# Performance work log

Hardware: AMD Instinct MI355X
Metric: run time of the kernel (lower is better)

The kernel has to match this reference:

```python
import jax, jax.numpy as jnp
import numpy as np

WEIGHT_SCALE = 0.02  # matches torch.randn(...)*0.02 init

def setup_inputs() -> dict:
    key = jax.random.key(0)
    k1, k2, k3, k4 = jax.random.split(key, 4)
    B, D = 16384, 1024
    x_re = jax.random.normal(k1, (B, D), dtype=jnp.float32)
    x_im = jax.random.normal(k2, (B, D), dtype=jnp.float32)
    w_re = jax.random.normal(k3, (D, D), dtype=jnp.float32) * WEIGHT_SCALE
    w_im = jax.random.normal(k4, (D, D), dtype=jnp.float32) * WEIGHT_SCALE
    return {"x_re": x_re, "x_im": x_im, "w_re": w_re, "w_im": w_im}

def reference(x_re, x_im, w_re, w_im):
    x = jax.lax.complex(x_re, x_im)            # [B, D] complex64
    W = jax.lax.complex(w_re, w_im)            # [D, D] complex64
    # Skew-Hermitian part: A = W - W^H
    A = W - jnp.conj(W.T)
    D = W.shape[0]
    I = jnp.eye(D, dtype=W.dtype)
    # Cayley transform: U = (I - A)^{-1} (I + A)  (unitary)
    U = jnp.linalg.solve(I - A, I + A)
    # Original: x @ U.transpose(-1, -2) (plain transpose, no conj)
    return x @ U.T
```

## Files before the change

### kernel.cpp

```cpp
#include <hip/hip_runtime.h>
#include <hip/hip_bf16.h>

#define DD 1024
#define NB 16384
#define SZ (DD * DD)
#define CHB 256

typedef unsigned short u16;
typedef __attribute__((ext_vector_type(2))) float f32x2;
typedef __attribute__((ext_vector_type(4))) float f32x4;
typedef __attribute__((ext_vector_type(8))) short short8;
typedef __attribute__((ext_vector_type(4))) short short4v;

__device__ __forceinline__ u16 f32_bf16(float f) {
  unsigned u = __builtin_bit_cast(unsigned, f);
  u += 0x7FFFu + ((u >> 16) & 1u);
  return (u16)(u >> 16);
}
__device__ __forceinline__ float bf16_f32(u16 h) {
  unsigned u = ((unsigned)h) << 16;
  return __builtin_bit_cast(float, u);
}
__device__ __forceinline__ void gload16(const void* g, void* l) {
  __builtin_amdgcn_global_load_lds(
      (const __attribute__((address_space(1))) unsigned int*)g,
      (__attribute__((address_space(3))) unsigned int*)l, 16, 0, 0);
}

struct CArgs {
  const u16 *Ar[3], *Ai[3];
  const u16 *Br[3], *Bi[3];
  int nseg;
  float alpha, g1, g2, ddiag;
  const u16 *e1r, *e1i, *e2r, *e2i;
  u16 *hi_n_re, *hi_n_im, *lo_n_re, *lo_n_im;
  u16 *t1_re, *t1_im;
  u16 *t2_re, *t2_im;
  u16 *lt_re, *lt_im;
  int t_ldt;
  unsigned t1_xi;
  const float *cxr, *cxi; u16 *cxb;
  int cm0a, cm1a, cm0b, cm1b;
};

__global__ __launch_bounds__(256, 2) void zchain(CArgs g) {
  constexpr int SA = 64 * 32, SB = 64 * 32;
  constexpr int SLOT = 2 * SA + 2 * SB;
  __shared__ __align__(16) u16 smem[4 * SLOT];
  const int tid = threadIdx.x;

  if ((int)blockIdx.x >= CHB) {
    int nra = g.cm1a - g.cm0a;
    int tot = nra + (g.cm1b - g.cm0b);
    for (int r = (int)blockIdx.x - CHB; r < tot; r += 256) {
      int m = (r < nra) ? (g.cm0a + r) : (g.cm0b + r - nra);
      f32x4 v = ((const f32x4*)g.cxr)[m * 256 + tid];
      short4v s;
      #pragma unroll
      for (int e = 0; e < 4; ++e) s[e] = (short)f32_bf16(v[e]);
      ((short4v*)g.cxb)[m * 512 + tid] = s;
      f32x4 w = ((const f32x4*)g.cxi)[m * 256 + tid];
      #pragma unroll
      for (int e = 0; e < 4; ++e) s[e] = (short)f32_bf16(w[e]);
      ((short4v*)g.cxb)[m * 512 + 256 + tid] = s;
    }
    return;
  }

  const int lane = tid & 63, wave = tid >> 6;
  const int wr = wave >> 1, wc = wave & 1;
  const int l15 = lane & 15, lg = lane >> 4;

  const int lin = blockIdx.x;
  const int xcd = lin & 7, tt = lin >> 3;
  const int by = (xcd >> 1) * 4 + (tt >> 3);
  const int bx = (xcd & 1) * 8 + (tt & 7);
  const int m0 = by * 64, n0 = bx * 64;

  const int arow = tid >> 2, agc = tid & 3;
  const int offA = (m0 + arow) * DD + ((agc ^ ((arow >> 1) & 3)) * 8);
  const int offB = (n0 + arow) * DD + ((agc ^ ((arow >> 1) & 3)) * 8);
  const int ldsAB = tid * 8;

  const int slotR = lg ^ ((l15 >> 1) & 3);
  int frA[2], frB[2];
  #pragma unroll
  for (int mf = 0; mf < 2; ++mf)
    frA[mf] = (wr * 32 + mf * 16 + l15) * 32 + slotR * 8;
  #pragma unroll
  for (int nf = 0; nf < 2; ++nf)
    frB[nf] = (wc * 32 + nf * 16 + l15) * 32 + slotR * 8;

  const int nt = g.nseg * 32;

  auto ISSUE = [&](int b) {
    if (b >= nt) return;
    int s = b >> 5, kk = (b & 31) << 5;
    u16* base = smem + (b & 3) * SLOT;
    gload16(g.Ar[s] + offA + kk, base + ldsAB);
    gload16(g.Ai[s] + offA + kk, base + SA + ldsAB);
    gload16(g.Br[s] + offB + kk, base + 2 * SA + ldsAB);
    gload16(g.Bi[s] + offB + kk, base + 2 * SA + SB + ldsAB);
  };

  f32x4 accre[2][2] = {};
  f32x4 accim[2][2] = {};

  ISSUE(0); ISSUE(1);
  asm volatile("s_waitcnt vmcnt(0)" ::: "memory");
  __builtin_amdgcn_s_barrier();

  for (int b = 0; b < nt; b += 2) {
    ISSUE(b + 2); ISSUE(b + 3);

    #pragma unroll
    for (int half = 0; half < 2; ++half) {
      const u16* base = smem + ((b + half) & 3) * SLOT;
      short8 ar[2], ai[2], br[2], bi[2], bin[2];
      #pragma unroll
      for (int mf = 0; mf < 2; ++mf) {
        ar[mf] = *(const short8*)(base + frA[mf]);
        ai[mf] = *(const short8*)(base + SA + frA[mf]);
      }
      #pragma unroll
      for (int nf = 0; nf < 2; ++nf) {
        br[nf] = *(const short8*)(base + 2 * SA + frB[nf]);
        bi[nf] = *(const short8*)(base + 2 * SA + SB + frB[nf]);
        #pragma unroll
        for (int e = 0; e < 8; ++e) bin[nf][e] = (short)(bi[nf][e] ^ (short)0x8000);
      }
      __builtin_amdgcn_s_setprio(1);
      #pragma unroll
      for (int mf = 0; mf < 2; ++mf)
      #pragma unroll
      for (int nf = 0; nf < 2; ++nf) {
        accre[mf][nf] = __builtin_amdgcn_mfma_f32_16x16x32_bf16(ar[mf], br[nf],  accre[mf][nf], 0, 0, 0);
        accre[mf][nf] = __builtin_amdgcn_mfma_f32_16x16x32_bf16(ai[mf], bin[nf], accre[mf][nf], 0, 0, 0);
        accim[mf][nf] = __builtin_amdgcn_mfma_f32_16x16x32_bf16(ar[mf], bi[nf],  accim[mf][nf], 0, 0, 0);
        accim[mf][nf] = __builtin_amdgcn_mfma_f32_16x16x32_bf16(ai[mf], br[nf],  accim[mf][nf], 0, 0, 0);
      }
      __builtin_amdgcn_s_setprio(0);
    }

    if (b + 2 < nt) {
      asm volatile("s_waitcnt vmcnt(0)" ::: "memory");
      __builtin_amdgcn_s_barrier();
    }
  }

  u16 hre[2][2][4], hie[2][2][4], lre[2][2][4], lie[2][2][4];
  #pragma unroll
  for (int mf = 0; mf < 2; ++mf)
  #pragma unroll
  for (int nf = 0; nf < 2; ++nf)
  #pragma unroll
  for (int r = 0; r < 4; ++r) {
    int gr = m0 + wr * 32 + mf * 16 + lg * 4 + r;
    int gc = n0 + wc * 32 + nf * 16 + l15;
    size_t idx = (size_t)gr * DD + gc;
    float v = g.alpha * accre[mf][nf][r];
    float w = g.alpha * accim[mf][nf][r];
    if (g.e1r) { v += g.g1 * bf16_f32(g.e1r[idx]); w += g.g1 * bf16_f32(g.e1i[idx]); }
    if (g.e2r) { v += g.g2 * bf16_f32(g.e2r[idx]); w += g.g2 * bf16_f32(g.e2i[idx]); }
    if (gr == gc) v += g.ddiag;
    u16 h1 = f32_bf16(v); hre[mf][nf][r] = h1;
    u16 h2 = f32_bf16(w); hie[mf][nf][r] = h2;
    lre[mf][nf][r] = f32_bf16(v - bf16_f32(h1));
    lie[mf][nf][r] = f32_bf16(w - bf16_f32(h2));
    if (g.hi_n_re) { g.hi_n_re[idx] = h1; g.hi_n_im[idx] = h2; }
    if (g.lo_n_re) { g.lo_n_re[idx] = lre[mf][nf][r]; g.lo_n_im[idx] = lie[mf][nf][r]; }
  }

  auto bounce = [&](u16 (&vals)[2][2][4], u16* outp, unsigned xorm) {
    if (!outp) return;
    __syncthreads();
    #pragma unroll
    for (int mf = 0; mf < 2; ++mf)
    #pragma unroll
    for (int nf = 0; nf < 2; ++nf)
    #pragma unroll
    for (int r = 0; r < 4; ++r) {
      int row = wr * 32 + mf * 16 + lg * 4 + r;
      int col = wc * 32 + nf * 16 + l15;
      smem[row * 66 + col] = vals[mf][nf][r];
    }
    __syncthreads();
    {
      int col = tid & 63, mb = (tid >> 6) * 16;
      short8 s0, s1;
      #pragma unroll
      for (int j = 0; j < 8; ++j) s0[j] = (short)(smem[(mb + j) * 66 + col] ^ xorm);
      #pragma unroll
      for (int j = 0; j < 8; ++j) s1[j] = (short)(smem[(mb + 8 + j) * 66 + col] ^ xorm);
      u16* p = outp + (size_t)(n0 + col) * g.t_ldt + m0 + mb;
      *(short8*)p = s0; *(short8*)(p + 8) = s1;
    }
  };

  bounce(hre, g.t1_re, 0);
  bounce(hie, g.t1_im, g.t1_xi);
  bounce(hre, g.t2_re, 0);
  bounce(hie, g.t2_im, 0);
  bounce(lre, g.lt_re, 0);
  bounce(lie, g.lt_im, 0);
}

#define RG_SLOT2 (2 * 256 * 64)
#define RG_LDS_BYTES (2 * RG_SLOT2 * 2)
#define RG_TILES 32

__global__ __launch_bounds__(512, 2) void rgemm(
    const u16* __restrict__ A, const u16* __restrict__ B,
    float* __restrict__ out, int ostride, int ooff)
{
  extern __shared__ u16 smem[];
  const int tid = threadIdx.x, lane = tid & 63, wave = tid >> 6;
  const int wr = wave >> 2, wc = wave & 3;
  const int l15 = lane & 15, lg = lane >> 4;

  int bx, by;
  { int lin = blockIdx.y * gridDim.x + blockIdx.x;
    int orig = (lin & 7) * 32 + (lin >> 3);
    bx = orig & 3; by = orig >> 2; }
  const int m0 = by * 256, n0 = bx * 256;

  const u16* __restrict__ Abase = A + (size_t)m0 * 2048;
  const u16* __restrict__ Bbase = B + (size_t)n0 * 2048;

  int gofsA[2], gofsB[2], lofs[2];
  #pragma unroll
  for (int i = 0; i < 2; ++i) {
    int c = i * 512 + tid;
    int sub = c >> 3;
    int sl = (c & 7) ^ (sub & 7);
    int rowA = (sub & 63) + 128 * (sub >> 6);
    int rowB = (sub & 31) + 64 * (sub >> 5);
    gofsA[i] = rowA * 2048 + sl * 8;
    gofsB[i] = rowB * 2048 + sl * 8;
    lofs[i] = c * 8;
  }

  int raf[8], rbf[8];
  #pragma unroll
  for (int mf = 0; mf < 4; ++mf)
    #pragma unroll
    for (int k = 0; k < 2; ++k)
      raf[mf * 2 + k] = (wr * 64 + mf * 16 + l15) * 64 +
                        (((k * 4 + lg) ^ (l15 & 7)) * 8);
  #pragma unroll
  for (int nf = 0; nf < 2; ++nf)
    #pragma unroll
    for (int k = 0; k < 2; ++k)
      rbf[nf * 2 + k] = (wc * 32 + nf * 16 + l15) * 64 +
                        (((k * 4 + lg) ^ (l15 & 7)) * 8);

  f32x4 acc[8][4] = {};
  short8 aA[8], bb[8];

#define MFMA_Q(mb, nb)                                                        \
  _Pragma("unroll")                                                           \
  for (int mf = 0; mf < 4; ++mf)                                              \
    _Pragma("unroll")                                                         \
    for (int nf = 0; nf < 2; ++nf)                                            \
      _Pragma("unroll")                                                       \
      for (int k = 0; k < 2; ++k)                                             \
        acc[(mb) + mf][(nb) + nf] = __builtin_amdgcn_mfma_f32_16x16x32_bf16(  \
            aA[mf * 2 + k], bb[((nb) + nf) * 2 + k], acc[(mb) + mf][(nb) + nf], 0, 0, 0);

  {
    gload16(Abase + gofsA[0], smem + lofs[0]);
    gload16(Abase + gofsA[1], smem + lofs[1]);
    gload16(Bbase + gofsB[0], smem + 16384 + lofs[0]);
    gload16(Bbase + gofsB[1], smem + 16384 + lofs[1]);
    gload16(Bbase + gofsB[0] + 32 * 2048, smem + 16384 + 8192 + lofs[0]);
    gload16(Bbase + gofsB[1] + 32 * 2048, smem + 16384 + 8192 + lofs[1]);
    gload16(Abase + gofsA[0] + 64 * 2048, smem + 8192 + lofs[0]);
    gload16(Abase + gofsA[1] + 64 * 2048, smem + 8192 + lofs[1]);
    gload16(Abase + gofsA[0] + 64, smem + RG_SLOT2 + lofs[0]);
    gload16(Abase + gofsA[1] + 64, smem + RG_SLOT2 + lofs[1]);
    gload16(Bbase + gofsB[0] + 64, smem + RG_SLOT2 + 16384 + lofs[0]);
    gload16(Bbase + gofsB[1] + 64, smem + RG_SLOT2 + 16384 + lofs[1]);
  }
  asm volatile("s_waitcnt vmcnt(4)" ::: "memory");
  __builtin_amdgcn_s_barrier();

  auto TILE = [&](int t, int gate, bool st01, bool st23) {
    const int b = t & 1;
    const u16* bA = smem + b * RG_SLOT2;
    const u16* bB = bA + 16384;
    u16* sOpp  = smem + (b ^ 1) * RG_SLOT2;
    u16* sSame = smem + b * RG_SLOT2;
    #pragma unroll
    for (int i = 0; i < 8; ++i) aA[i] = *(const short8*)(bA + raf[i]);
    #pragma unroll
    for (int i = 0; i < 4; ++i) bb[i] = *(const short8*)(bB + rbf[i]);
    if (st01) {
      int kk = (t + 1) * 64;
      gload16(Bbase + gofsB[0] + 32 * 2048 + kk, sOpp + 16384 + 8192 + lofs[0]);
      gload16(Bbase + gofsB[1] + 32 * 2048 + kk, sOpp + 16384 + 8192 + lofs[1]);
    }
    asm volatile("s_waitcnt lgkmcnt(8)" ::: "memory");
    __builtin_amdgcn_s_barrier();
    asm volatile("s_waitcnt lgkmcnt(0)" ::: "memory");
    __builtin_amdgcn_sched_barrier(0);
    __builtin_amdgcn_s_setprio(1);
    MFMA_Q(0, 0);
    __builtin_amdgcn_s_setprio(0);
    __builtin_amdgcn_s_barrier();
    #pragma unroll
    for (int i = 0; i < 4; ++i) bb[4 + i] = *(const short8*)(bB + 8192 + rbf[i]);
    if (st01) {
      int kk = (t + 1) * 64;
      gload16(Abase + gofsA[0] + 64 * 2048 + kk, sOpp + 8192 + lofs[0]);
      gload16(Abase + gofsA[1] + 64 * 2048 + kk, sOpp + 8192 + lofs[1]);
    }
    __builtin_amdgcn_s_barrier();
    asm volatile("s_waitcnt lgkmcnt(0)" ::: "memory");
    __builtin_amdgcn_sched_barrier(0);
    __builtin_amdgcn_s_setprio(1);
    MFMA_Q(0, 2);
    __builtin_amdgcn_s_setprio(0);
    __builtin_amdgcn_s_barrier();
    #pragma unroll
    for (int i = 0; i < 8; ++i) aA[i] = *(const short8*)(bA + 8192 + raf[i]);
    if (st23) {
      int kk = (t + 2) * 64;
      gload16(Abase + gofsA[0] + kk, sSame + lofs[0]);
      gload16(Abase + gofsA[1] + kk, sSame + lofs[1]);
    }
    __builtin_amdgcn_s_barrier();
    asm volatile("s_waitcnt lgkmcnt(0)" ::: "memory");
    __builtin_amdgcn_sched_barrier(0);
    __builtin_amdgcn_s_setprio(1);
    MFMA_Q(4, 0);
    __builtin_amdgcn_s_setprio(0);
    __builtin_amdgcn_s_barrier();
    if (st23) {
      int kk = (t + 2) * 64;
      gload16(Bbase + gofsB[0] + kk, sSame + 16384 + lofs[0]);
      gload16(Bbase + gofsB[1] + kk, sSame + 16384 + lofs[1]);
    }
    __builtin_amdgcn_s_barrier();
    __builtin_amdgcn_sched_barrier(0);
    __builtin_amdgcn_s_setprio(1);
    MFMA_Q(4, 2);
    __builtin_amdgcn_s_setprio(0);
    if (gate == 4)      asm volatile("s_waitcnt vmcnt(4)" ::: "memory");
    else if (gate == 0) asm volatile("s_waitcnt vmcnt(0)" ::: "memory");
    if (gate >= 0) __builtin_amdgcn_s_barrier();
  };

  for (int t = 0; t < RG_TILES - 2; ++t) TILE(t, 4, true, true);
  TILE(RG_TILES - 2, 0, true, false);
  TILE(RG_TILES - 1, -1, false, false);
#undef MFMA_Q

  #pragma unroll
  for (int mf = 0; mf < 8; ++mf)
  #pragma unroll
  for (int nf = 0; nf < 4; ++nf)
  #pragma unroll
  for (int r = 0; r < 4; ++r) {
    int gr = m0 + wr * 128 + mf * 16 + lg * 4 + r;
    int gc = n0 + wc * 64 + nf * 16 + l15;
    out[((size_t)gr * DD + gc) * ostride + ooff] = acc[mf][nf][r];
  }
}

__global__ __launch_bounds__(256) void prep_w(
    const float* __restrict__ wre, const float* __restrict__ wim,
    u16* Shr, u16* Shi_, u16* Slr, u16* Sli, u16* Snr)
{
  __shared__ float tr[32][33], ti[32][33];
  const int tx = threadIdx.x, ty = threadIdx.y;
  const int bx = blockIdx.x, by = blockIdx.y;
  #pragma unroll
  for (int k = 0; k < 4; ++k) {
    int r = bx * 32 + ty + 8 * k, c = by * 32 + tx;
    tr[ty + 8 * k][tx] = wre[r * DD + c];
    ti[ty + 8 * k][tx] = wim[r * DD + c];
  }
  __syncthreads();
  #pragma unroll
  for (int k = 0; k < 4; ++k) {
    int i = by * 32 + ty + 8 * k, j = bx * 32 + tx;
    float wr_ij = wre[i * DD + j], wi_ij = wim[i * DD + j];
    float wr_ji = tr[tx][ty + 8 * k], wi_ji = ti[tx][ty + 8 * k];
    float Sre = wr_ji - wr_ij;
    float Sim = wi_ij + wi_ji;
    int idx = i * DD + j;
    u16 h1 = f32_bf16(Sre); Shr[idx] = h1; Slr[idx] = f32_bf16(Sre - bf16_f32(h1));
    u16 h2 = f32_bf16(Sim); Shi_[idx] = h2; Sli[idx] = f32_bf16(Sim - bf16_f32(h2));
    Snr[idx] = (u16)(h1 ^ 0x8000u);
  }
}

__global__ __launch_bounds__(256) void prep_x2(
    const float* __restrict__ xr, const float* __restrict__ xi,
    u16* __restrict__ xb, int m0a, int m1a, int m0b, int m1b)
{
  int nra = m1a - m0a;
  int tot = nra + (m1b - m0b);
  const int tid = threadIdx.x;
  for (int r = blockIdx.x; r < tot; r += gridDim.x) {
    int m = (r < nra) ? (m0a + r) : (m0b + r - nra);
    f32x4 v = ((const f32x4*)xr)[m * 256 + tid];
    short4v s;
    #pragma unroll
    for (int e = 0; e < 4; ++e) s[e] = (short)f32_bf16(v[e]);
    ((short4v*)xb)[m * 512 + tid] = s;
    f32x4 w = ((const f32x4*)xi)[m * 256 + tid];
    #pragma unroll
    for (int e = 0; e < 4; ++e) s[e] = (short)f32_bf16(w[e]);
    ((short4v*)xb)[m * 512 + 256 + tid] = s;
  }
}

extern "C" void kernel_launch(void* const* d_in, const int* in_sizes, int n_in,
                              void* d_out, int out_size, void* d_ws, size_t ws_size,
                              hipStream_t stream)
{
  const float* xr  = (const float*)d_in[0];
  const float* xi  = (const float*)d_in[1];
  const float* wre = (const float*)d_in[2];
  const float* wim = (const float*)d_in[3];
  const bool realOut = (out_size == NB * DD);

  u16* P0 = (u16*)d_ws;
  auto PL = [&](int k) { return P0 + (size_t)k * SZ; };
  u16 *Shr = PL(0), *Shi_ = PL(1), *Slr = PL(2), *Sli = PL(3), *Snr = PL(4);
  u16 *Cn_r = PL(5), *Cn_i = PL(6), *Ct_r = PL(7), *Ct_i = PL(8);
  u16 *Rn_r = PL(9), *Rn_i = PL(10);
  u16 *XA_hn_r = PL(11), *XA_hn_i = PL(12), *XA_ht_r = PL(13), *XA_ht_i = PL(14);
  u16 *XB_hn_r = PL(19), *XB_hn_i = PL(20), *XB_ht_r = PL(21), *XB_ht_i = PL(22);
  u16 *XB_ln_r = PL(23), *XB_ln_i = PL(24), *XB_lt_r = PL(25), *XB_lt_i = PL(26);
  u16 *T_ht_r = PL(29), *T_ht_i = PL(30), *T_lt_r = PL(31), *T_lt_i = PL(32);
  u16 *pack1 = PL(33);
  u16 *pack2 = PL(35);
  u16 *xb    = PL(0);

  dim3 blk(256);
  prep_w<<<dim3(32, 32), dim3(32, 8), 0, stream>>>(
      wre, wim, Shr, Shi_, Slr, Sli, Snr);

  auto chain = [&](CArgs& a, int p0, int p1, int p0b, int p1b) {
    a.cxr = xr; a.cxi = xi; a.cxb = xb;
    a.cm0a = p0 * 512; a.cm1a = p1 * 512;
    a.cm0b = p0b * 512; a.cm1b = p1b * 512;
    zchain<<<dim3(CHB + 256), blk, 0, stream>>>(a);
  };
  auto base = [&]() { CArgs a{}; a.nseg = 1; a.t_ldt = DD; return a; };

  { CArgs a = base();
    a.Ar[0] = Shr; a.Ai[0] = Shi_; a.Br[0] = Snr; a.Bi[0] = Shi_;
    a.alpha = 1.f;
    a.hi_n_re = Cn_r; a.hi_n_im = Cn_i; a.t1_re = Ct_r; a.t1_im = Ct_i;
    chain(a, 15, 19, 0, 0); }
  { CArgs a = base();
    a.Ar[0] = Cn_r; a.Ai[0] = Cn_i; a.Br[0] = Ct_r; a.Bi[0] = Ct_i;
    a.alpha = 0.0212604f; a.g1 = 0.2381155f; a.e1r = Cn_r; a.e1i = Cn_i;
    a.ddiag = 0.7910964f;
    a.hi_n_re = Rn_r; a.hi_n_im = Rn_i;
    chain(a, 27, 29, 0, 0); }
  { CArgs a = base();
    a.Ar[0] = Rn_r; a.Ai[0] = Rn_i; a.Br[0] = Snr; a.Bi[0] = Shi_;
    a.alpha = 1.f; a.g1 = 1.f; a.e1r = Rn_r; a.e1i = Rn_i;
    a.hi_n_re = XA_hn_r; a.hi_n_im = XA_hn_i; a.t1_re = XA_ht_r; a.t1_im = XA_ht_i;
    chain(a, 0, 0, 0, 0); }
  { CArgs a = base();
    a.Ar[0] = Shr; a.Ai[0] = Shi_; a.Br[0] = XA_ht_r; a.Bi[0] = XA_ht_i;
    a.alpha = -1.f; a.g1 = 1.f; a.e1r = XA_hn_r; a.e1i = XA_hn_i;
    a.t1_re = T_ht_r; a.t1_im = T_ht_i;
    chain(a, 4, 8, 0, 0); }
  { CArgs a = base();
    a.Ar[0] = XA_hn_r; a.Ai[0] = XA_hn_i; a.Br[0] = T_ht_r; a.Bi[0] = T_ht_i;
    a.alpha = -1.f; a.g1 = 2.f; a.e1r = XA_hn_r; a.e1i = XA_hn_i;
    a.hi_n_re = XB_hn_r; a.hi_n_im = XB_hn_i; a.t1_re = XB_ht_r; a.t1_im = XB_ht_i;
    a.lo_n_re = XB_ln_r; a.lo_n_im = XB_ln_i; a.lt_re = XB_lt_r; a.lt_im = XB_lt_i;
    chain(a, 8, 11, 0, 0); }
  { CArgs a = base();
    a.nseg = 3;
    a.Ar[0] = Shr; a.Ai[0] = Shi_; a.Br[0] = XB_ht_r; a.Bi[0] = XB_ht_i;
    a.Ar[1] = Shr; a.Ai[1] = Shi_; a.Br[1] = XB_lt_r; a.Bi[1] = XB_lt_i;
    a.Ar[2] = Slr; a.Ai[2] = Sli;  a.Br[2] = XB_ht_r; a.Bi[2] = XB_ht_i;
    a.alpha = -1.f;
    a.g1 = 1.f; a.e1r = XB_hn_r; a.e1i = XB_hn_i;
    a.g2 = 1.f; a.e2r = XB_ln_r; a.e2i = XB_ln_i;
    a.t1_re = T_ht_r; a.t1_im = T_ht_i; a.lt_re = T_lt_r; a.lt_im = T_lt_i;
    chain(a, 11, 15, 0, 0); }
  { CArgs a = base();
    a.nseg = 2;
    a.Ar[0] = XB_hn_r; a.Ai[0] = XB_hn_i; a.Br[0] = T_ht_r; a.Bi[0] = T_ht_i;
    a.Ar[1] = XB_hn_r; a.Ai[1] = XB_hn_i; a.Br[1] = T_lt_r; a.Bi[1] = T_lt_i;
    a.alpha = -2.f;
    a.g1 = 4.f; a.e1r = XB_hn_r; a.e1i = XB_hn_i;
    a.g2 = 2.f; a.e2r = XB_ln_r; a.e2i = XB_ln_i;
    a.ddiag = -1.f;
    a.t_ldt = 2048;
    a.t1_re = pack1; a.t1_im = pack1 + 1024; a.t1_xi = 0x8000u;
    if (!realOut) { a.t2_im = pack2; a.t2_re = pack2 + 1024; }
    chain(a, 0, 4, 0, 0); }

  prep_x2<<<dim3(1024), blk, 0, stream>>>(
      xr, xi, xb, 19 * 512, 27 * 512, 29 * 512, 32 * 512);

  (void)hipFuncSetAttribute((const void*)rgemm,
      hipFuncAttributeMaxDynamicSharedMemorySize, RG_LDS_BYTES);
  dim3 gB(DD / 256, NB / 256);
  if (realOut) {
    rgemm<<<gB, dim3(512), RG_LDS_BYTES, stream>>>(xb, pack1, (float*)d_out, 1, 0);
  } else {
    rgemm<<<gB, dim3(512), RG_LDS_BYTES, stream>>>(xb, pack1, (float*)d_out, 2, 0);
    rgemm<<<gB, dim3(512), RG_LDS_BYTES, stream>>>(xb, pack2, (float*)d_out, 2, 1);
  }
}
```

Before: 288.1 us.

## Split K across two wave groups in zchain with LDS reduction

The zchain complex GEMM blocks go from 256 to 512 threads. Two groups of four waves each handle half the K range with their own double-buffered LDS slots, and the partial accumulators are then summed through shared memory before the epilogue. The side blocks that convert x to bf16 now put the real and imaginary halves on separate thread halves. The aim is more waves in flight per block to hide latency in these small 64x64-tile GEMMs. In exchange it adds a cross-group LDS reduction and an extra barrier, shortens the prefetch depth per group, and may lower occupancy because of the larger blocks.

```diff
diff --git a/kernel.cpp b/kernel.cpp
--- a/kernel.cpp
+++ b/kernel.cpp
@@ -43,7 +43,7 @@
   int cm0a, cm1a, cm0b, cm1b;
 };
 
-__global__ __launch_bounds__(256, 2) void zchain(CArgs g) {
+__global__ __launch_bounds__(512, 2) void zchain(CArgs g) {
   constexpr int SA = 64 * 32, SB = 64 * 32;
   constexpr int SLOT = 2 * SA + 2 * SB;
   __shared__ __align__(16) u16 smem[4 * SLOT];
@@ -52,23 +52,22 @@
   if ((int)blockIdx.x >= CHB) {
     int nra = g.cm1a - g.cm0a;
     int tot = nra + (g.cm1b - g.cm0b);
+    const int chalf = tid >> 8, ct = tid & 255;
+    const float* csrc = chalf ? g.cxi : g.cxr;
     for (int r = (int)blockIdx.x - CHB; r < tot; r += 256) {
       int m = (r < nra) ? (g.cm0a + r) : (g.cm0b + r - nra);
-      f32x4 v = ((const f32x4*)g.cxr)[m * 256 + tid];
+      f32x4 v = ((const f32x4*)csrc)[m * 256 + ct];
       short4v s;
       #pragma unroll
       for (int e = 0; e < 4; ++e) s[e] = (short)f32_bf16(v[e]);
-      ((short4v*)g.cxb)[m * 512 + tid] = s;
-      f32x4 w = ((const f32x4*)g.cxi)[m * 256 + tid];
-      #pragma unroll
-      for (int e = 0; e < 4; ++e) s[e] = (short)f32_bf16(w[e]);
-      ((short4v*)g.cxb)[m * 512 + 256 + tid] = s;
+      ((short4v*)g.cxb)[m * 512 + chalf * 256 + ct] = s;
     }
     return;
   }
 
   const int lane = tid & 63, wave = tid >> 6;
-  const int wr = wave >> 1, wc = wave & 1;
+  const int kh = wave >> 2;
+  const int wr = (wave >> 1) & 1, wc = wave & 1;
   const int l15 = lane & 15, lg = lane >> 4;
 
   const int lin = blockIdx.x;
@@ -77,10 +76,11 @@
   const int bx = (xcd & 1) * 8 + (tt & 7);
   const int m0 = by * 64, n0 = bx * 64;
 
-  const int arow = tid >> 2, agc = tid & 3;
+  const int t8 = tid & 255;
+  const int arow = t8 >> 2, agc = t8 & 3;
   const int offA = (m0 + arow) * DD + ((agc ^ ((arow >> 1) & 3)) * 8);
   const int offB = (n0 + arow) * DD + ((agc ^ ((arow >> 1) & 3)) * 8);
-  const int ldsAB = tid * 8;
+  const int ldsAB = t8 * 8;
 
   const int slotR = lg ^ ((l15 >> 1) & 3);
   int frA[2], frB[2];
@@ -91,12 +91,13 @@
   for (int nf = 0; nf < 2; ++nf)
     frB[nf] = (wc * 32 + nf * 16 + l15) * 32 + slotR * 8;
 
-  const int nt = g.nseg * 32;
+  const int ntH = g.nseg * 16;
 
   auto ISSUE = [&](int b) {
-    if (b >= nt) return;
-    int s = b >> 5, kk = (b & 31) << 5;
-    u16* base = smem + (b & 3) * SLOT;
+    if (b >= ntH) return;
+    int k = kh * ntH + b;
+    int s = k >> 5, kk = (k & 31) << 5;
+    u16* base = smem + (kh * 2 + (b & 1)) * SLOT;
     gload16(g.Ar[s] + offA + kk, base + ldsAB);
     gload16(g.Ai[s] + offA + kk, base + SA + ldsAB);
     gload16(g.Br[s] + offB + kk, base + 2 * SA + ldsAB);
@@ -106,94 +107,115 @@
   f32x4 accre[2][2] = {};
   f32x4 accim[2][2] = {};
 
-  ISSUE(0); ISSUE(1);
+  ISSUE(0);
   asm volatile("s_waitcnt vmcnt(0)" ::: "memory");
   __builtin_amdgcn_s_barrier();
 
-  for (int b = 0; b < nt; b += 2) {
-    ISSUE(b + 2); ISSUE(b + 3);
-
-    #pragma unroll
-    for (int half = 0; half < 2; ++half) {
-      const u16* base = smem + ((b + half) & 3) * SLOT;
-      short8 ar[2], ai[2], br[2], bi[2], bin[2];
+  for (int b = 0; b < ntH; ++b) {
+    ISSUE(b + 1);
+    const u16* base = smem + (kh * 2 + (b & 1)) * SLOT;
+    short8 ar[2], ai[2], br[2], bi[2], bin[2];
+    #pragma unroll
+    for (int mf = 0; mf < 2; ++mf) {
+      ar[mf] = *(const short8*)(base + frA[mf]);
+      ai[mf] = *(const short8*)(base + SA + frA[mf]);
+    }
+    #pragma unroll
+    for (int nf = 0; nf < 2; ++nf) {
+      br[nf] = *(const short8*)(base + 2 * SA + frB[nf]);
+      bi[nf] = *(const short8*)(base + 2 * SA + SB + frB[nf]);
       #pragma unroll
-      for (int mf = 0; mf < 2; ++mf) {
-        ar[mf] = *(const short8*)(base + frA[mf]);
-        ai[mf] = *(const short8*)(base + SA + frA[mf]);
-      }
-      #pragma unroll
-      for (int nf = 0; nf < 2; ++nf) {
-        br[nf] = *(const short8*)(base + 2 * SA + frB[nf]);
-        bi[nf] = *(const short8*)(base + 2 * SA + SB + frB[nf]);
-        #pragma unroll
-        for (int e = 0; e < 8; ++e) bin[nf][e] = (short)(bi[nf][e] ^ (short)0x8000);
-      }
-      __builtin_amdgcn_s_setprio(1);
+      for (int e = 0; e < 8; ++e) bin[nf][e] = (short)(bi[nf][e] ^ (short)0x8000);
+    }
+    __builtin_amdgcn_s_setprio(1);
+    #pragma unroll
+    for (int mf = 0; mf < 2; ++mf)
+    #pragma unroll
+    for (int nf = 0; nf < 2; ++nf) {
+      accre[mf][nf] = __builtin_amdgcn_mfma_f32_16x16x32_bf16(ar[mf], br[nf],  accre[mf][nf], 0, 0, 0);
+      accre[mf][nf] = __builtin_amdgcn_mfma_f32_16x16x32_bf16(ai[mf], bin[nf], accre[mf][nf], 0, 0, 0);
+      accim[mf][nf] = __builtin_amdgcn_mfma_f32_16x16x32_bf16(ar[mf], bi[nf],  accim[mf][nf], 0, 0, 0);
+      accim[mf][nf] = __builtin_amdgcn_mfma_f32_16x16x32_bf16(ai[mf], br[nf],  accim[mf][nf], 0, 0, 0);
+    }
+    __builtin_amdgcn_s_setprio(0);
+    asm volatile("s_waitcnt vmcnt(0)" ::: "memory");
+    __builtin_amdgcn_s_barrier();
+  }
+
+  {
+    float* cbuf = (float*)(smem + 16384);
+    const int ci = (((wave & 3) << 6) + lane) * 4;
+    if (kh) {
+      *(f32x4*)(cbuf + 0 * 1024 + ci) = accre[0][0];
+      *(f32x4*)(cbuf + 1 * 1024 + ci) = accre[0][1];
+      *(f32x4*)(cbuf + 2 * 1024 + ci) = accre[1][0];
+      *(f32x4*)(cbuf + 3 * 1024 + ci) = accre[1][1];
+      *(f32x4*)(cbuf + 4 * 1024 + ci) = accim[0][0];
+      *(f32x4*)(cbuf + 5 * 1024 + ci) = accim[0][1];
+      *(f32x4*)(cbuf + 6 * 1024 + ci) = accim[1][0];
+      *(f32x4*)(cbuf + 7 * 1024 + ci) = accim[1][1];
+    }
+    __syncthreads();
+    if (!kh) {
+      accre[0][0] += *(const f32x4*)(cbuf + 0 * 1024 + ci);
+      accre[0][1] += *(const f32x4*)(cbuf + 1 * 1024 + ci);
+      accre[1][0] += *(const f32x4*)(cbuf + 2 * 1024 + ci);
+      accre[1][1] += *(const f32x4*)(cbuf + 3 * 1024 + ci);
+      accim[0][0] += *(const f32x4*)(cbuf + 4 * 1024 + ci);
+      accim[0][1] += *(const f32x4*)(cbuf + 5 * 1024 + ci);
+      accim[1][0] += *(const f32x4*)(cbuf + 6 * 1024 + ci);
+      accim[1][1] += *(const f32x4*)(cbuf + 7 * 1024 + ci);
+    }
+  }
+
+  u16 hre[2][2][4], hie[2][2][4], lre[2][2][4], lie[2][2][4];
+  if (tid < 256) {
+    #pragma unroll
+    for (int mf = 0; mf < 2; ++mf)
+    #pragma unroll
+    for (int nf = 0; nf < 2; ++nf)
+    #pragma unroll
+    for (int r = 0; r < 4; ++r) {
+      int gr = m0 + wr * 32 + mf * 16 + lg * 4 + r;
+      int gc = n0 + wc * 32 + nf * 16 + l15;
+      size_t idx = (size_t)gr * DD + gc;
+      float v = g.alpha * accre[mf][nf][r];
+      float w = g.alpha * accim[mf][nf][r];
+      if (g.e1r) { v += g.g1 * bf16_f32(g.e1r[idx]); w += g.g1 * bf16_f32(g.e1i[idx]); }
+      if (g.e2r) { v += g.g2 * bf16_f32(g.e2r[idx]); w += g.g2 * bf16_f32(g.e2i[idx]); }
+      if (gr == gc) v += g.ddiag;
+      u16 h1 = f32_bf16(v); hre[mf][nf][r] = h1;
+      u16 h2 = f32_bf16(w); hie[mf][nf][r] = h2;
+      lre[mf][nf][r] = f32_bf16(v - bf16_f32(h1));
+      lie[mf][nf][r] = f32_bf16(w - bf16_f32(h2));
+      if (g.hi_n_re) { g.hi_n_re[idx] = h1; g.hi_n_im[idx] = h2; }
+      if (g.lo_n_re) { g.lo_n_re[idx] = lre[mf][nf][r]; g.lo_n_im[idx] = lie[mf][nf][r]; }
+    }
+  }
+
+  auto bounce = [&](u16 (&vals)[2][2][4], u16* outp, unsigned xorm) {
+    if (!outp) return;
+    __syncthreads();
+    if (tid < 256) {
       #pragma unroll
       for (int mf = 0; mf < 2; ++mf)
       #pragma unroll
-      for (int nf = 0; nf < 2; ++nf) {
-        accre[mf][nf] = __builtin_amdgcn_mfma_f32_16x16x32_bf16(ar[mf], br[nf],  accre[mf][nf], 0, 0, 0);
-        accre[mf][nf] = __builtin_amdgcn_mfma_f32_16x16x32_bf16(ai[mf], bin[nf], accre[mf][nf], 0, 0, 0);
-        accim[mf][nf] = __builtin_amdgcn_mfma_f32_16x16x32_bf16(ar[mf], bi[nf],  accim[mf][nf], 0, 0, 0);
-        accim[mf][nf] = __builtin_amdgcn_mfma_f32_16x16x32_bf16(ai[mf], br[nf],  accim[mf][nf], 0, 0, 0);
+      for (int nf = 0; nf < 2; ++nf)
+      #pragma unroll
+      for (int r = 0; r < 4; ++r) {
+        int row = wr * 32 + mf * 16 + lg * 4 + r;
+        int col = wc * 32 + nf * 16 + l15;
+        smem[row * 66 + col] = vals[mf][nf][r];
       }
-      __builtin_amdgcn_s_setprio(0);
-    }
-
-    if (b + 2 < nt) {
-      asm volatile("s_waitcnt vmcnt(0)" ::: "memory");
-      __builtin_amdgcn_s_barrier();
-    }
-  }
-
-  u16 hre[2][2][4], hie[2][2][4], lre[2][2][4], lie[2][2][4];
-  #pragma unroll
-  for (int mf = 0; mf < 2; ++mf)
-  #pragma unroll
-  for (int nf = 0; nf < 2; ++nf)
-  #pragma unroll
-  for (int r = 0; r < 4; ++r) {
-    int gr = m0 + wr * 32 + mf * 16 + lg * 4 + r;
-    int gc = n0 + wc * 32 + nf * 16 + l15;
-    size_t idx = (size_t)gr * DD + gc;
-    float v = g.alpha * accre[mf][nf][r];
-    float w = g.alpha * accim[mf][nf][r];
-    if (g.e1r) { v += g.g1 * bf16_f32(g.e1r[idx]); w += g.g1 * bf16_f32(g.e1i[idx]); }
-    if (g.e2r) { v += g.g2 * bf16_f32(g.e2r[idx]); w += g.g2 * bf16_f32(g.e2i[idx]); }
-    if (gr == gc) v += g.ddiag;
-    u16 h1 = f32_bf16(v); hre[mf][nf][r] = h1;
-    u16 h2 = f32_bf16(w); hie[mf][nf][r] = h2;
-    lre[mf][nf][r] = f32_bf16(v - bf16_f32(h1));
-    lie[mf][nf][r] = f32_bf16(w - bf16_f32(h2));
-    if (g.hi_n_re) { g.hi_n_re[idx] = h1; g.hi_n_im[idx] = h2; }
-    if (g.lo_n_re) { g.lo_n_re[idx] = lre[mf][nf][r]; g.lo_n_im[idx] = lie[mf][nf][r]; }
-  }
-
-  auto bounce = [&](u16 (&vals)[2][2][4], u16* outp, unsigned xorm) {
-    if (!outp) return;
-    __syncthreads();
-    #pragma unroll
-    for (int mf = 0; mf < 2; ++mf)
-    #pragma unroll
-    for (int nf = 0; nf < 2; ++nf)
-    #pragma unroll
-    for (int r = 0; r < 4; ++r) {
-      int row = wr * 32 + mf * 16 + lg * 4 + r;
-      int col = wc * 32 + nf * 16 + l15;
-      smem[row * 66 + col] = vals[mf][nf][r];
     }
     __syncthreads();
     {
-      int col = tid & 63, mb = (tid >> 6) * 16;
-      short8 s0, s1;
+      int col = tid & 63, mb = (tid >> 6) * 8;
+      short8 s0;
       #pragma unroll
       for (int j = 0; j < 8; ++j) s0[j] = (short)(smem[(mb + j) * 66 + col] ^ xorm);
-      #pragma unroll
-      for (int j = 0; j < 8; ++j) s1[j] = (short)(smem[(mb + 8 + j) * 66 + col] ^ xorm);
       u16* p = outp + (size_t)(n0 + col) * g.t_ldt + m0 + mb;
-      *(short8*)p = s0; *(short8*)(p + 8) = s1;
+      *(short8*)p = s0;
     }
   };
 
@@ -447,7 +469,7 @@
     a.cxr = xr; a.cxi = xi; a.cxb = xb;
     a.cm0a = p0 * 512; a.cm1a = p1 * 512;
     a.cm0b = p0b * 512; a.cm1b = p1b * 512;
-    zchain<<<dim3(CHB + 256), blk, 0, stream>>>(a);
+    zchain<<<dim3(CHB + 256), dim3(512), 0, stream>>>(a);
   };
   auto base = [&]() { CArgs a{}; a.nseg = 1; a.t_ldt = DD; return a; };
 
```

Result: slower. 302.3 us (+4.9%).

## Fuse seven chain GEMM launches and x conversion into one cooperative kernel

Applied to the files above, without the earlier changes.

Replaces the seven separate zchain launches and the prep_x2 launch with a single cooperative kernel that loops over the seven stages, separated by grid-wide syncs, and converts the remaining x rows at the end. The aim is to remove per-launch overhead and the idle gaps between the small dependent 1024x1024 GEMMs. In exchange, grid.sync carries its own cost, all 512 blocks must be co-resident, and the final x conversion is now serialized after the chain rather than running as its own launch.

```diff
diff --git a/kernel.cpp b/kernel.cpp
--- a/kernel.cpp
+++ b/kernel.cpp
@@ -1,5 +1,8 @@
 #include <hip/hip_runtime.h>
 #include <hip/hip_bf16.h>
+#include <hip/hip_cooperative_groups.h>
+
+namespace cg = cooperative_groups;
 
 #define DD 1024
 #define NB 16384
@@ -43,166 +46,188 @@
   int cm0a, cm1a, cm0b, cm1b;
 };
 
-__global__ __launch_bounds__(256, 2) void zchain(CArgs g) {
+struct MegaArgs { CArgs seg[7]; };
+
+__global__ __launch_bounds__(256, 2) void zfused(MegaArgs M) {
   constexpr int SA = 64 * 32, SB = 64 * 32;
   constexpr int SLOT = 2 * SA + 2 * SB;
   __shared__ __align__(16) u16 smem[4 * SLOT];
   const int tid = threadIdx.x;
-
-  if ((int)blockIdx.x >= CHB) {
-    int nra = g.cm1a - g.cm0a;
-    int tot = nra + (g.cm1b - g.cm0b);
-    for (int r = (int)blockIdx.x - CHB; r < tot; r += 256) {
-      int m = (r < nra) ? (g.cm0a + r) : (g.cm0b + r - nra);
-      f32x4 v = ((const f32x4*)g.cxr)[m * 256 + tid];
-      short4v s;
-      #pragma unroll
-      for (int e = 0; e < 4; ++e) s[e] = (short)f32_bf16(v[e]);
-      ((short4v*)g.cxb)[m * 512 + tid] = s;
-      f32x4 w = ((const f32x4*)g.cxi)[m * 256 + tid];
-      #pragma unroll
-      for (int e = 0; e < 4; ++e) s[e] = (short)f32_bf16(w[e]);
-      ((short4v*)g.cxb)[m * 512 + 256 + tid] = s;
-    }
-    return;
-  }
+  const int bid = (int)blockIdx.x;
+  cg::grid_group grid = cg::this_grid();
 
   const int lane = tid & 63, wave = tid >> 6;
   const int wr = wave >> 1, wc = wave & 1;
   const int l15 = lane & 15, lg = lane >> 4;
-
-  const int lin = blockIdx.x;
-  const int xcd = lin & 7, tt = lin >> 3;
+  const int xcd = bid & 7, tt = bid >> 3;
   const int by = (xcd >> 1) * 4 + (tt >> 3);
   const int bx = (xcd & 1) * 8 + (tt & 7);
   const int m0 = by * 64, n0 = bx * 64;
-
   const int arow = tid >> 2, agc = tid & 3;
   const int offA = (m0 + arow) * DD + ((agc ^ ((arow >> 1) & 3)) * 8);
   const int offB = (n0 + arow) * DD + ((agc ^ ((arow >> 1) & 3)) * 8);
   const int ldsAB = tid * 8;
-
   const int slotR = lg ^ ((l15 >> 1) & 3);
-  int frA[2], frB[2];
+  int frA[2];
   #pragma unroll
   for (int mf = 0; mf < 2; ++mf)
     frA[mf] = (wr * 32 + mf * 16 + l15) * 32 + slotR * 8;
+  int frB[2];
   #pragma unroll
   for (int nf = 0; nf < 2; ++nf)
     frB[nf] = (wc * 32 + nf * 16 + l15) * 32 + slotR * 8;
 
-  const int nt = g.nseg * 32;
-
-  auto ISSUE = [&](int b) {
-    if (b >= nt) return;
-    int s = b >> 5, kk = (b & 31) << 5;
-    u16* base = smem + (b & 3) * SLOT;
-    gload16(g.Ar[s] + offA + kk, base + ldsAB);
-    gload16(g.Ai[s] + offA + kk, base + SA + ldsAB);
-    gload16(g.Br[s] + offB + kk, base + 2 * SA + ldsAB);
-    gload16(g.Bi[s] + offB + kk, base + 2 * SA + SB + ldsAB);
-  };
-
-  f32x4 accre[2][2] = {};
-  f32x4 accim[2][2] = {};
-
-  ISSUE(0); ISSUE(1);
-  asm volatile("s_waitcnt vmcnt(0)" ::: "memory");
-  __builtin_amdgcn_s_barrier();
-
-  for (int b = 0; b < nt; b += 2) {
-    ISSUE(b + 2); ISSUE(b + 3);
-
-    #pragma unroll
-    for (int half = 0; half < 2; ++half) {
-      const u16* base = smem + ((b + half) & 3) * SLOT;
-      short8 ar[2], ai[2], br[2], bi[2], bin[2];
-      #pragma unroll
-      for (int mf = 0; mf < 2; ++mf) {
-        ar[mf] = *(const short8*)(base + frA[mf]);
-        ai[mf] = *(const short8*)(base + SA + frA[mf]);
+  for (int s7 = 0; s7 < 7; ++s7) {
+    const CArgs& g = M.seg[s7];
+
+    if (bid >= CHB) {
+      int nra = g.cm1a - g.cm0a;
+      int tot = nra + (g.cm1b - g.cm0b);
+      for (int r = bid - CHB; r < tot; r += 256) {
+        int m = (r < nra) ? (g.cm0a + r) : (g.cm0b + r - nra);
+        f32x4 v = ((const f32x4*)g.cxr)[m * 256 + tid];
+        short4v s;
+        #pragma unroll
+        for (int e = 0; e < 4; ++e) s[e] = (short)f32_bf16(v[e]);
+        ((short4v*)g.cxb)[m * 512 + tid] = s;
+        f32x4 w = ((const f32x4*)g.cxi)[m * 256 + tid];
+        #pragma unroll
+        for (int e = 0; e < 4; ++e) s[e] = (short)f32_bf16(w[e]);
+        ((short4v*)g.cxb)[m * 512 + 256 + tid] = s;
       }
-      #pragma unroll
-      for (int nf = 0; nf < 2; ++nf) {
-        br[nf] = *(const short8*)(base + 2 * SA + frB[nf]);
-        bi[nf] = *(const short8*)(base + 2 * SA + SB + frB[nf]);
+    } else {
+      const int nt = g.nseg * 32;
+
+      auto ISSUE = [&](int b) {
+        if (b >= nt) return;
+        int s = b >> 5, kk = (b & 31) << 5;
+        u16* base = smem + (b & 3) * SLOT;
+        gload16(g.Ar[s] + offA + kk, base + ldsAB);
+        gload16(g.Ai[s] + offA + kk, base + SA + ldsAB);
+        gload16(g.Br[s] + offB + kk, base + 2 * SA + ldsAB);
+        gload16(g.Bi[s] + offB + kk, base + 2 * SA + SB + ldsAB);
+      };
+
+      f32x4 accre[2][2] = {};
+      f32x4 accim[2][2] = {};
+
+      ISSUE(0); ISSUE(1);
+      asm volatile("s_waitcnt vmcnt(0)" ::: "memory");
+      __builtin_amdgcn_s_barrier();
+
+      for (int b = 0; b < nt; b += 2) {
+        ISSUE(b + 2); ISSUE(b + 3);
         #pragma unroll
-        for (int e = 0; e < 8; ++e) bin[nf][e] = (short)(bi[nf][e] ^ (short)0x8000);
+        for (int h2 = 0; h2 < 2; ++h2) {
+          const u16* base = smem + ((b + h2) & 3) * SLOT;
+          short8 ar[2], ai[2], br[2], bi[2], bin[2];
+          #pragma unroll
+          for (int mf = 0; mf < 2; ++mf) {
+            ar[mf] = *(const short8*)(base + frA[mf]);
+            ai[mf] = *(const short8*)(base + SA + frA[mf]);
+          }
+          #pragma unroll
+          for (int nf = 0; nf < 2; ++nf) {
+            br[nf] = *(const short8*)(base + 2 * SA + frB[nf]);
+            bi[nf] = *(const short8*)(base + 2 * SA + SB + frB[nf]);
+            #pragma unroll
+            for (int e = 0; e < 8; ++e) bin[nf][e] = (short)(bi[nf][e] ^ (short)0x8000);
+          }
+          __builtin_amdgcn_s_setprio(1);
+          #pragma unroll
+          for (int mf = 0; mf < 2; ++mf)
+          #pragma unroll
+          for (int nf = 0; nf < 2; ++nf) {
+            accre[mf][nf] = __builtin_amdgcn_mfma_f32_16x16x32_bf16(ar[mf], br[nf],  accre[mf][nf], 0, 0, 0);
+            accre[mf][nf] = __builtin_amdgcn_mfma_f32_16x16x32_bf16(ai[mf], bin[nf], accre[mf][nf], 0, 0, 0);
+            accim[mf][nf] = __builtin_amdgcn_mfma_f32_16x16x32_bf16(ar[mf], bi[nf],  accim[mf][nf], 0, 0, 0);
+            accim[mf][nf] = __builtin_amdgcn_mfma_f32_16x16x32_bf16(ai[mf], br[nf],  accim[mf][nf], 0, 0, 0);
+          }
+          __builtin_amdgcn_s_setprio(0);
+        }
+        if (b + 2 < nt) {
+          asm volatile("s_waitcnt vmcnt(0)" ::: "memory");
+          __builtin_amdgcn_s_barrier();
+        }
       }
-      __builtin_amdgcn_s_setprio(1);
+
+      u16 hre[2][2][4], hie[2][2][4], lre[2][2][4], lie[2][2][4];
       #pragma unroll
       for (int mf = 0; mf < 2; ++mf)
       #pragma unroll
-      for (int nf = 0; nf < 2; ++nf) {
-        accre[mf][nf] = __builtin_amdgcn_mfma_f32_16x16x32_bf16(ar[mf], br[nf],  accre[mf][nf], 0, 0, 0);
-        accre[mf][nf] = __builtin_amdgcn_mfma_f32_16x16x32_bf16(ai[mf], bin[nf], accre[mf][nf], 0, 0, 0);
-        accim[mf][nf] = __builtin_amdgcn_mfma_f32_16x16x32_bf16(ar[mf], bi[nf],  accim[mf][nf], 0, 0, 0);
-        accim[mf][nf] = __builtin_amdgcn_mfma_f32_16x16x32_bf16(ai[mf], br[nf],  accim[mf][nf], 0, 0, 0);
+      for (int nf = 0; nf < 2; ++nf)
+      #pragma unroll
+      for (int r = 0; r < 4; ++r) {
+        int gr = m0 + wr * 32 + mf * 16 + lg * 4 + r;
+        int gc = n0 + wc * 32 + nf * 16 + l15;
+        size_t idx = (size_t)gr * DD + gc;
+        float v = g.alpha * accre[mf][nf][r];
+        float w = g.alpha * accim[mf][nf][r];
+        if (g.e1r) { v += g.g1 * bf16_f32(g.e1r[idx]); w += g.g1 * bf16_f32(g.e1i[idx]); }
+        if (g.e2r) { v += g.g2 * bf16_f32(g.e2r[idx]); w += g.g2 * bf16_f32(g.e2i[idx]); }
+        if (gr == gc) v += g.ddiag;
+        u16 h1 = f32_bf16(v); hre[mf][nf][r] = h1;
+        u16 h2 = f32_bf16(w); hie[mf][nf][r] = h2;
+        lre[mf][nf][r] = f32_bf16(v - bf16_f32(h1));
+        lie[mf][nf][r] = f32_bf16(w - bf16_f32(h2));
+        if (g.hi_n_re) { g.hi_n_re[idx] = h1; g.hi_n_im[idx] = h2; }
+        if (g.lo_n_re) { g.lo_n_re[idx] = lre[mf][nf][r]; g.lo_n_im[idx] = lie[mf][nf][r]; }
       }
-      __builtin_amdgcn_s_setprio(0);
+
+      auto bounce = [&](u16 (&vals)[2][2][4], u16* outp, unsigned xorm) {
+        if (!outp) return;
+        __syncthreads();
+        #pragma unroll
+        for (int mf = 0; mf < 2; ++mf)
+        #pragma unroll
+        for (int nf = 0; nf < 2; ++nf)
+        #pragma unroll
+        for (int r = 0; r < 4; ++r) {
+          int row = wr * 32 + mf * 16 + lg * 4 + r;
+          int col = wc * 32 + nf * 16 + l15;
+          smem[row * 66 + col] = vals[mf][nf][r];
+        }
+        __syncthreads();
+        {
+          int col = tid & 63, mb = (tid >> 6) * 16;
+          short8 s0, s1;
+          #pragma unroll
+          for (int j = 0; j < 8; ++j) s0[j] = (short)(smem[(mb + j) * 66 + col] ^ xorm);
+          #pragma unroll
+          for (int j = 0; j < 8; ++j) s1[j] = (short)(smem[(mb + 8 + j) * 66 + col] ^ xorm);
+          u16* p = outp + (size_t)(n0 + col) * g.t_ldt + m0 + mb;
+          *(short8*)p = s0; *(short8*)(p + 8) = s1;
+        }
+      };
+
+      bounce(hre, g.t1_re, 0);
+      bounce(hie, g.t1_im, g.t1_xi);
+      bounce(hre, g.t2_re, 0);
+      bounce(hie, g.t2_im, 0);
+      bounce(lre, g.lt_re, 0);
+      bounce(lie, g.lt_im, 0);
     }
 
-    if (b + 2 < nt) {
-      asm volatile("s_waitcnt vmcnt(0)" ::: "memory");
-      __builtin_amdgcn_s_barrier();
+    grid.sync();
+  }
+
+  {
+    const float* xr = M.seg[0].cxr;
+    const float* xi = M.seg[0].cxi;
+    u16* xb = M.seg[0].cxb;
+    for (int r = bid; r < 5632; r += CHB + 256) {
+      int m = (r < 4096) ? (19 * 512 + r) : (29 * 512 + (r - 4096));
+      f32x4 v = ((const f32x4*)xr)[m * 256 + tid];
+      short4v s;
+      #pragma unroll
+      for (int e = 0; e < 4; ++e) s[e] = (short)f32_bf16(v[e]);
+      ((short4v*)xb)[m * 512 + tid] = s;
+      f32x4 w = ((const f32x4*)xi)[m * 256 + tid];
+      #pragma unroll
+      for (int e = 0; e < 4; ++e) s[e] = (short)f32_bf16(w[e]);
+      ((short4v*)xb)[m * 512 + 256 + tid] = s;
     }
   }
-
-  u16 hre[2][2][4], hie[2][2][4], lre[2][2][4], lie[2][2][4];
-  #pragma unroll
-  for (int mf = 0; mf < 2; ++mf)
-  #pragma unroll
-  for (int nf = 0; nf < 2; ++nf)
-  #pragma unroll
-  for (int r = 0; r < 4; ++r) {
-    int gr = m0 + wr * 32 + mf * 16 + lg * 4 + r;
-    int gc = n0 + wc * 32 + nf * 16 + l15;
-    size_t idx = (size_t)gr * DD + gc;
-    float v = g.alpha * accre[mf][nf][r];
-    float w = g.alpha * accim[mf][nf][r];
-    if (g.e1r) { v += g.g1 * bf16_f32(g.e1r[idx]); w += g.g1 * bf16_f32(g.e1i[idx]); }
-    if (g.e2r) { v += g.g2 * bf16_f32(g.e2r[idx]); w += g.g2 * bf16_f32(g.e2i[idx]); }
-    if (gr == gc) v += g.ddiag;
-    u16 h1 = f32_bf16(v); hre[mf][nf][r] = h1;
-    u16 h2 = f32_bf16(w); hie[mf][nf][r] = h2;
-    lre[mf][nf][r] = f32_bf16(v - bf16_f32(h1));
-    lie[mf][nf][r] = f32_bf16(w - bf16_f32(h2));
-    if (g.hi_n_re) { g.hi_n_re[idx] = h1; g.hi_n_im[idx] = h2; }
-    if (g.lo_n_re) { g.lo_n_re[idx] = lre[mf][nf][r]; g.lo_n_im[idx] = lie[mf][nf][r]; }
-  }
-
-  auto bounce = [&](u16 (&vals)[2][2][4], u16* outp, unsigned xorm) {
-    if (!outp) return;
-    __syncthreads();
-    #pragma unroll
-    for (int mf = 0; mf < 2; ++mf)
-    #pragma unroll
-    for (int nf = 0; nf < 2; ++nf)
-    #pragma unroll
-    for (int r = 0; r < 4; ++r) {
-      int row = wr * 32 + mf * 16 + lg * 4 + r;
-      int col = wc * 32 + nf * 16 + l15;
-      smem[row * 66 + col] = vals[mf][nf][r];
-    }
-    __syncthreads();
-    {
-      int col = tid & 63, mb = (tid >> 6) * 16;
-      short8 s0, s1;
-      #pragma unroll
-      for (int j = 0; j < 8; ++j) s0[j] = (short)(smem[(mb + j) * 66 + col] ^ xorm);
-      #pragma unroll
-      for (int j = 0; j < 8; ++j) s1[j] = (short)(smem[(mb + 8 + j) * 66 + col] ^ xorm);
-      u16* p = outp + (size_t)(n0 + col) * g.t_ldt + m0 + mb;
-      *(short8*)p = s0; *(short8*)(p + 8) = s1;
-    }
-  };
-
-  bounce(hre, g.t1_re, 0);
-  bounce(hie, g.t1_im, g.t1_xi);
-  bounce(hre, g.t2_re, 0);
-  bounce(hie, g.t2_im, 0);
-  bounce(lre, g.lt_re, 0);
-  bounce(lie, g.lt_im, 0);
 }
 
 #define RG_SLOT2 (2 * 256 * 64)
@@ -395,27 +420,6 @@
   }
 }
 
-__global__ __launch_bounds__(256) void prep_x2(
-    const float* __restrict__ xr, const float* __restrict__ xi,
-    u16* __restrict__ xb, int m0a, int m1a, int m0b, int m1b)
-{
-  int nra = m1a - m0a;
-  int tot = nra + (m1b - m0b);
-  const int tid = threadIdx.x;
-  for (int r = blockIdx.x; r < tot; r += gridDim.x) {
-    int m = (r < nra) ? (m0a + r) : (m0b + r - nra);
-    f32x4 v = ((const f32x4*)xr)[m * 256 + tid];
-    short4v s;
-    #pragma unroll
-    for (int e = 0; e < 4; ++e) s[e] = (short)f32_bf16(v[e]);
-    ((short4v*)xb)[m * 512 + tid] = s;
-    f32x4 w = ((const f32x4*)xi)[m * 256 + tid];
-    #pragma unroll
-    for (int e = 0; e < 4; ++e) s[e] = (short)f32_bf16(w[e]);
-    ((short4v*)xb)[m * 512 + 256 + tid] = s;
-  }
-}
-
 extern "C" void kernel_launch(void* const* d_in, const int* in_sizes, int n_in,
                               void* d_out, int out_size, void* d_ws, size_t ws_size,
                               hipStream_t stream)
@@ -439,15 +443,16 @@
   u16 *pack2 = PL(35);
   u16 *xb    = PL(0);
 
-  dim3 blk(256);
   prep_w<<<dim3(32, 32), dim3(32, 8), 0, stream>>>(
       wre, wim, Shr, Shi_, Slr, Sli, Snr);
 
-  auto chain = [&](CArgs& a, int p0, int p1, int p0b, int p1b) {
+  MegaArgs M{};
+  int segi = 0;
+  auto seg = [&](CArgs& a, int p0, int p1, int p0b, int p1b) {
     a.cxr = xr; a.cxi = xi; a.cxb = xb;
     a.cm0a = p0 * 512; a.cm1a = p1 * 512;
     a.cm0b = p0b * 512; a.cm1b = p1b * 512;
-    zchain<<<dim3(CHB + 256), blk, 0, stream>>>(a);
+    M.seg[segi++] = a;
   };
   auto base = [&]() { CArgs a{}; a.nseg = 1; a.t_ldt = DD; return a; };
 
@@ -455,29 +460,29 @@
     a.Ar[0] = Shr; a.Ai[0] = Shi_; a.Br[0] = Snr; a.Bi[0] = Shi_;
     a.alpha = 1.f;
     a.hi_n_re = Cn_r; a.hi_n_im = Cn_i; a.t1_re = Ct_r; a.t1_im = Ct_i;
-    chain(a, 15, 19, 0, 0); }
+    seg(a, 15, 19, 0, 0); }
   { CArgs a = base();
     a.Ar[0] = Cn_r; a.Ai[0] = Cn_i; a.Br[0] = Ct_r; a.Bi[0] = Ct_i;
     a.alpha = 0.0212604f; a.g1 = 0.2381155f; a.e1r = Cn_r; a.e1i = Cn_i;
     a.ddiag = 0.7910964f;
     a.hi_n_re = Rn_r; a.hi_n_im = Rn_i;
-    chain(a, 27, 29, 0, 0); }
+    seg(a, 27, 29, 0, 0); }
   { CArgs a = base();
     a.Ar[0] = Rn_r; a.Ai[0] = Rn_i; a.Br[0] = Snr; a.Bi[0] = Shi_;
     a.alpha = 1.f; a.g1 = 1.f; a.e1r = Rn_r; a.e1i = Rn_i;
     a.hi_n_re = XA_hn_r; a.hi_n_im = XA_hn_i; a.t1_re = XA_ht_r; a.t1_im = XA_ht_i;
-    chain(a, 0, 0, 0, 0); }
+    seg(a, 0, 0, 0, 0); }
   { CArgs a = base();
     a.Ar[0] = Shr; a.Ai[0] = Shi_; a.Br[0] = XA_ht_r; a.Bi[0] = XA_ht_i;
     a.alpha = -1.f; a.g1 = 1.f; a.e1r = XA_hn_r; a.e1i = XA_hn_i;
     a.t1_re = T_ht_r; a.t1_im = T_ht_i;
-    chain(a, 4, 8, 0, 0); }
+    seg(a, 4, 8, 0, 0); }
   { CArgs a = base();
     a.Ar[0] = XA_hn_r; a.Ai[0] = XA_hn_i; a.Br[0] = T_ht_r; a.Bi[0] = T_ht_i;
     a.alpha = -1.f; a.g1 = 2.f; a.e1r = XA_hn_r; a.e1i = XA_hn_i;
     a.hi_n_re = XB_hn_r; a.hi_n_im = XB_hn_i; a.t1_re = XB_ht_r; a.t1_im = XB_ht_i;
     a.lo_n_re = XB_ln_r; a.lo_n_im = XB_ln_i; a.lt_re = XB_lt_r; a.lt_im = XB_lt_i;
-    chain(a, 8, 11, 0, 0); }
+    seg(a, 8, 11, 0, 0); }
   { CArgs a = base();
     a.nseg = 3;
     a.Ar[0] = Shr; a.Ai[0] = Shi_; a.Br[0] = XB_ht_r; a.Bi[0] = XB_ht_i;
@@ -487,7 +492,7 @@
     a.g1 = 1.f; a.e1r = XB_hn_r; a.e1i = XB_hn_i;
     a.g2 = 1.f; a.e2r = XB_ln_r; a.e2i = XB_ln_i;
     a.t1_re = T_ht_r; a.t1_im = T_ht_i; a.lt_re = T_lt_r; a.lt_im = T_lt_i;
-    chain(a, 11, 15, 0, 0); }
+    seg(a, 11, 15, 0, 0); }
   { CArgs a = base();
     a.nseg = 2;
     a.Ar[0] = XB_hn_r; a.Ai[0] = XB_hn_i; a.Br[0] = T_ht_r; a.Bi[0] = T_ht_i;
@@ -499,10 +504,13 @@
     a.t_ldt = 2048;
     a.t1_re = pack1; a.t1_im = pack1 + 1024; a.t1_xi = 0x8000u;
     if (!realOut) { a.t2_im = pack2; a.t2_re = pack2 + 1024; }
-    chain(a, 0, 4, 0, 0); }
-
-  prep_x2<<<dim3(1024), blk, 0, stream>>>(
-      xr, xi, xb, 19 * 512, 27 * 512, 29 * 512, 32 * 512);
+    seg(a, 0, 4, 0, 0); }
+
+  {
+    void* kargs[] = {(void*)&M};
+    (void)hipLaunchCooperativeKernel((const void*)zfused,
+        dim3(CHB + 256), dim3(256), kargs, 0, stream);
+  }
 
   (void)hipFuncSetAttribute((const void*)rgemm,
       hipFuncAttributeMaxDynamicSharedMemorySize, RG_LDS_BYTES);
```

Measured after the change: 740.7 us. 157% more time.
